# Optimization experiments

Hardware: AMD Instinct MI355X
Metric: run time of the kernel (lower is better)

Reference implementation:

```python
import jax, jax.numpy as jnp
import numpy as np

XYZ_MIN = -1.0
XYZ_MAX = 1.0
ALPHA_INIT = 1e-6
ACT_SHIFT = float(np.log(1.0 / (1.0 - ALPHA_INIT) - 1.0))  # density bias shift


def trilinear_sample(grid, xyz):
    """PyTorch F.grid_sample(mode='bilinear', align_corners=True) for 3D.
    grid: [C, D, H, W] (D<->z, H<->y, W<->x); xyz: [N,3] global coords in [XYZ_MIN, XYZ_MAX].
    Returns [N, C]."""
    C, D, H, W = grid.shape
    u = (xyz - XYZ_MIN) / (XYZ_MAX - XYZ_MIN)            # [N,3] in [0,1]
    sizes = jnp.array([W, H, D], dtype=xyz.dtype)
    pos = u * (sizes - 1.0)                               # align_corners=True mapping
    i0f = jnp.floor(pos)
    w1 = pos - i0f                                        # [N,3] frac weights
    w0 = 1.0 - w1
    maxi = jnp.array([W - 1, H - 1, D - 1], dtype=jnp.int32)
    i0 = jnp.clip(i0f.astype(jnp.int32), 0, maxi)
    i1 = jnp.minimum(i0 + 1, maxi)
    x0, y0, z0 = i0[:, 0], i0[:, 1], i0[:, 2]
    x1, y1, z1 = i1[:, 0], i1[:, 1], i1[:, 2]
    gf = grid.reshape(C, -1)                              # [C, D*H*W]

    def corner(z, y, x):
        lin = (z * H + y) * W + x                         # [N]
        return gf[:, lin]                                 # [C, N]

    wx0, wy0, wz0 = w0[:, 0], w0[:, 1], w0[:, 2]
    wx1, wy1, wz1 = w1[:, 0], w1[:, 1], w1[:, 2]
    out = (corner(z0, y0, x0) * (wz0 * wy0 * wx0)
           + corner(z0, y0, x1) * (wz0 * wy0 * wx1)
           + corner(z0, y1, x0) * (wz0 * wy1 * wx0)
           + corner(z0, y1, x1) * (wz0 * wy1 * wx1)
           + corner(z1, y0, x0) * (wz1 * wy0 * wx0)
           + corner(z1, y0, x1) * (wz1 * wy0 * wx1)
           + corner(z1, y1, x0) * (wz1 * wy1 * wx0)
           + corner(z1, y1, x1) * (wz1 * wy1 * wx1))
    return out.T                                          # [N, C]


def setup_inputs() -> dict:
    key = jax.random.key(0)
    k1, k2, k3, k4, k5 = jax.random.split(key, 5)
    R, P = 16384, 256
    # Keep all sampled points inside [-1, 1]^3 (in-bounds grid_sample).
    origins = (jax.random.uniform(k1, (R, 3), jnp.float32) - 0.5) * 0.5   # [-0.25, 0.25]
    d = jax.random.normal(k2, (R, 3), jnp.float32)
    directions = d / jnp.linalg.norm(d, axis=-1, keepdims=True) * 0.5     # norm 0.5
    lengths = jax.random.uniform(k3, (R, P), jnp.float32)                 # [0, 1)
    density_grid = jax.random.normal(k4, (1, 160, 160, 160), jnp.float32) * 0.1
    color_grid = jax.random.normal(k5, (3, 160, 160, 160), jnp.float32) * 0.1
    return {"origins": origins, "directions": directions, "lengths": lengths,
            "density_grid": density_grid, "color_grid": color_grid}


def reference(origins, directions, lengths, density_grid, color_grid):
    R, P = lengths.shape
    # ray_bundle_to_ray_points: origins + directions * lengths
    pts = origins[:, None, :] + directions[:, None, :] * lengths[:, :, None]  # [R,P,3]
    interval = jnp.linalg.norm(directions, axis=-1)[:, None, None]            # [R,1,1]
    flat = pts.reshape(-1, 3)
    raw_density = trilinear_sample(density_grid, flat).reshape(R, P, 1)
    # alpha = 1 - (1 + exp(density + shift)) ** (-interval)
    density = 1.0 - (1.0 + jnp.exp(raw_density + ACT_SHIFT)) ** (-interval)
    raw_color = trilinear_sample(color_grid, flat).reshape(R, P, 3)
    color = jax.nn.sigmoid(raw_color)
    return density, color
```

## Files before the change

kernel.cpp:

```cpp
#include <hip/hip_runtime.h>
#include <math.h>

#define NRAYS 16384
#define NPTS  256
#define GS    160
#define GS3   (GS*GS*GS)

#define ACT_SHIFT (-13.815509557963774f)
#define LOG2E     (1.4426950408889634f)

typedef float floatx2 __attribute__((ext_vector_type(2)));

__device__ __forceinline__ unsigned int pack4fp8(float d, float r, float g, float b) {
    int w = __builtin_amdgcn_cvt_pk_fp8_f32(d, r, 0, false);
    w     = __builtin_amdgcn_cvt_pk_fp8_f32(g, b, w, true);
    return (unsigned int)w;
}

__device__ __forceinline__ void acc2(unsigned int w, float cw,
                                     floatx2& sdr, floatx2& sgb) {
    floatx2 dr = __builtin_amdgcn_cvt_pk_f32_fp8((int)w, false);
    floatx2 gb = __builtin_amdgcn_cvt_pk_f32_fp8((int)w, true);
    floatx2 cw2 = {cw, cw};
    sdr += dr * cw2;
    sgb += gb * cw2;
}

__global__ __launch_bounds__(256)
void repack_fp8quad_kernel(const float* __restrict__ dgrid,
                           const float* __restrict__ cgrid,
                           uint4* __restrict__ out)
{
    const int i = blockIdx.x * 256 + threadIdx.x;
    if (i >= GS3) return;
    const int x = i % GS;
    const int y = (i / GS) % GS;
    const int ox = (x < GS - 1) ? 1  : 0;
    const int oy = (y < GS - 1) ? GS : 0;

    const int i00 = i, i10 = i + oy, i01 = i + ox, i11 = i + oy + ox;

    uint4 v;
    v.x = pack4fp8(dgrid[i00], cgrid[i00], cgrid[GS3 + i00], cgrid[2*GS3 + i00]);
    v.y = pack4fp8(dgrid[i10], cgrid[i10], cgrid[GS3 + i10], cgrid[2*GS3 + i10]);
    v.z = pack4fp8(dgrid[i01], cgrid[i01], cgrid[GS3 + i01], cgrid[2*GS3 + i01]);
    v.w = pack4fp8(dgrid[i11], cgrid[i11], cgrid[GS3 + i11], cgrid[2*GS3 + i11]);
    out[i] = v;
}

__global__ __launch_bounds__(256)
void sample_fp8_direct_kernel(const float* __restrict__ origins,
                              const float* __restrict__ directions,
                              const float* __restrict__ lengths,
                              const uint4* __restrict__ grid,
                              float* __restrict__ out_density,
                              float* __restrict__ out_color)
{
    const int r   = blockIdx.x;
    const int p   = threadIdx.x;
    const int idx = r * NPTS + p;

    const float t  = lengths[idx];
    const float ox = origins[3*r+0], oy = origins[3*r+1], oz = origins[3*r+2];
    const float dx = directions[3*r+0], dy = directions[3*r+1], dz = directions[3*r+2];
    const float interval = sqrtf(dx*dx + dy*dy + dz*dz);

    const float half_sm1 = 0.5f * (float)(GS - 1);
    const float px = (ox + dx*t + 1.0f) * half_sm1;
    const float py = (oy + dy*t + 1.0f) * half_sm1;
    const float pz = (oz + dz*t + 1.0f) * half_sm1;

    const float fx = floorf(px), fy = floorf(py), fz = floorf(pz);

    int x0 = min(max((int)fx, 0), GS-2);
    int y0 = min(max((int)fy, 0), GS-2);
    int z0 = min(max((int)fz, 0), GS-2);

    const int i0 = (z0*GS + y0)*GS + x0;

    const uint4 ez0 = grid[i0];
    const uint4 ez1 = grid[i0 + GS*GS];

    const float wx1 = px - fx, wy1 = py - fy, wz1 = pz - fz;
    const float wx0 = 1.0f - wx1, wy0 = 1.0f - wy1, wz0 = 1.0f - wz1;
    const float c00 = wy0*wx0, c10 = wy1*wx0, c01 = wy0*wx1, c11 = wy1*wx1;

    floatx2 sdr = {0.f, 0.f}, sgb = {0.f, 0.f};
    acc2(ez0.x, wz0*c00, sdr, sgb);
    acc2(ez0.y, wz0*c10, sdr, sgb);
    acc2(ez0.z, wz0*c01, sdr, sgb);
    acc2(ez0.w, wz0*c11, sdr, sgb);
    acc2(ez1.x, wz1*c00, sdr, sgb);
    acc2(ez1.y, wz1*c10, sdr, sgb);
    acc2(ez1.z, wz1*c01, sdr, sgb);
    acc2(ez1.w, wz1*c11, sdr, sgb);

    const float a  = sdr.x + ACT_SHIFT;
    const float ea = __builtin_amdgcn_exp2f(LOG2E * a);
    const float L  = __builtin_amdgcn_logf(1.0f + ea);
    out_density[idx] = 1.0f - __builtin_amdgcn_exp2f(-interval * L);

    const float e1 = __builtin_amdgcn_exp2f(-LOG2E * sdr.y);
    const float e2 = __builtin_amdgcn_exp2f(-LOG2E * sgb.x);
    const float e3 = __builtin_amdgcn_exp2f(-LOG2E * sgb.y);
    out_color[idx*3 + 0] = __builtin_amdgcn_rcpf(1.0f + e1);
    out_color[idx*3 + 1] = __builtin_amdgcn_rcpf(1.0f + e2);
    out_color[idx*3 + 2] = __builtin_amdgcn_rcpf(1.0f + e3);
}

__device__ __forceinline__ float2 ld2(const float* p) {
    return *reinterpret_cast<const float2*>(p);
}

__global__ __launch_bounds__(256)
void dvgo_render_kernel(const float* __restrict__ origins,
                        const float* __restrict__ directions,
                        const float* __restrict__ lengths,
                        const float* __restrict__ dgrid,
                        const float* __restrict__ cgrid,
                        float* __restrict__ out_density,
                        float* __restrict__ out_color)
{
    const int r = blockIdx.x;
    const int p = threadIdx.x;
    const int idx = r * NPTS + p;

    const float t  = lengths[idx];
    const float ox = origins[3*r+0], oy = origins[3*r+1], oz = origins[3*r+2];
    const float dx = directions[3*r+0], dy = directions[3*r+1], dz = directions[3*r+2];
    const float interval = sqrtf(dx*dx + dy*dy + dz*dz);

    const float x = ox + dx*t;
    const float y = oy + dy*t;
    const float z = oz + dz*t;

    const float half_sm1 = 0.5f * (float)(GS - 1);
    const float px = (x + 1.0f) * half_sm1;
    const float py = (y + 1.0f) * half_sm1;
    const float pz = (z + 1.0f) * half_sm1;

    const float fx = floorf(px), fy = floorf(py), fz = floorf(pz);
    const float wx1 = px - fx, wy1 = py - fy, wz1 = pz - fz;
    const float wx0 = 1.0f - wx1, wy0 = 1.0f - wy1, wz0 = 1.0f - wz1;

    int x0 = (int)fx, y0 = (int)fy, z0 = (int)fz;
    x0 = min(max(x0, 0), GS-2);
    y0 = min(max(y0, 0), GS-2);
    z0 = min(max(z0, 0), GS-2);

    int rows[4];
    rows[0] = ((z0  )*GS + y0  )*GS + x0;
    rows[1] = ((z0  )*GS + y0+1)*GS + x0;
    rows[2] = ((z0+1)*GS + y0  )*GS + x0;
    rows[3] = ((z0+1)*GS + y0+1)*GS + x0;

    const float* bases[4] = {dgrid, cgrid, cgrid + GS3, cgrid + 2*GS3};

    float2 v[4][4];
    #pragma unroll
    for (int ch = 0; ch < 4; ++ch)
        #pragma unroll
        for (int rr = 0; rr < 4; ++rr)
            v[ch][rr] = ld2(bases[ch] + rows[rr]);

    float rw[4];
    rw[0] = wz0*wy0; rw[1] = wz0*wy1; rw[2] = wz1*wy0; rw[3] = wz1*wy1;

    float s[4];
    #pragma unroll
    for (int ch = 0; ch < 4; ++ch) {
        float acc = 0.0f;
        #pragma unroll
        for (int rr = 0; rr < 4; ++rr)
            acc = fmaf(rw[rr], fmaf(v[ch][rr].x, wx0, v[ch][rr].y * wx1), acc);
        s[ch] = acc;
    }

    const float a  = s[0] + ACT_SHIFT;
    const float sp = (a > 20.0f) ? a : log1pf(__expf(a));
    out_density[idx] = 1.0f - __expf(-interval * sp);

    #pragma unroll
    for (int c = 0; c < 3; ++c)
        out_color[idx*3 + c] = 1.0f / (1.0f + __expf(-s[c+1]));
}

extern "C" void kernel_launch(void* const* d_in, const int* in_sizes, int n_in,
                              void* d_out, int out_size, void* d_ws, size_t ws_size,
                              hipStream_t stream) {
    const float* origins    = (const float*)d_in[0];
    const float* directions = (const float*)d_in[1];
    const float* lengths    = (const float*)d_in[2];
    const float* dgrid      = (const float*)d_in[3];
    const float* cgrid      = (const float*)d_in[4];

    float* out_density = (float*)d_out;
    float* out_color   = (float*)d_out + NRAYS*NPTS;

    if (ws_size >= (size_t)GS3 * sizeof(uint4)) {
        uint4* quads = (uint4*)d_ws;
        repack_fp8quad_kernel<<<(GS3 + 255) / 256, 256, 0, stream>>>(dgrid, cgrid, quads);
        sample_fp8_direct_kernel<<<NRAYS, NPTS, 0, stream>>>(
            origins, directions, lengths, quads, out_density, out_color);
    } else {
        dvgo_render_kernel<<<NRAYS, NPTS, 0, stream>>>(
            origins, directions, lengths, dgrid, cgrid, out_density, out_color);
    }
}
```

Before: 56.22 us.

## Repack grid as fp8 y-pairs and read x-neighbors with one 16-byte load

The repacked fp8 grid now stores only the voxel and its y+1 neighbor per entry, as 8 bytes, instead of a 16-byte quad that also held the x+1 neighbors. The sampler gets all four corners of a z-slice with one 16-byte load covering two adjacent entries. This halves both the repack write traffic and the workspace footprint, which should improve cache reuse during sampling. It also switches the lengths load and the output stores to nontemporal hints. The 16-byte loads are now only 8-byte aligned.

```diff
diff --git a/kernel.cpp b/kernel.cpp
--- a/kernel.cpp
+++ b/kernel.cpp
@@ -27,40 +27,34 @@
 }
 
 __global__ __launch_bounds__(256)
-void repack_fp8quad_kernel(const float* __restrict__ dgrid,
-                           const float* __restrict__ cgrid,
-                           uint4* __restrict__ out)
+void repack_fp8ypair_kernel(const float* __restrict__ dgrid,
+                            const float* __restrict__ cgrid,
+                            uint2* __restrict__ out)
 {
     const int i = blockIdx.x * 256 + threadIdx.x;
     if (i >= GS3) return;
-    const int x = i % GS;
-    const int y = (i / GS) % GS;
-    const int ox = (x < GS - 1) ? 1  : 0;
-    const int oy = (y < GS - 1) ? GS : 0;
-
-    const int i00 = i, i10 = i + oy, i01 = i + ox, i11 = i + oy + ox;
-
-    uint4 v;
-    v.x = pack4fp8(dgrid[i00], cgrid[i00], cgrid[GS3 + i00], cgrid[2*GS3 + i00]);
-    v.y = pack4fp8(dgrid[i10], cgrid[i10], cgrid[GS3 + i10], cgrid[2*GS3 + i10]);
-    v.z = pack4fp8(dgrid[i01], cgrid[i01], cgrid[GS3 + i01], cgrid[2*GS3 + i01]);
-    v.w = pack4fp8(dgrid[i11], cgrid[i11], cgrid[GS3 + i11], cgrid[2*GS3 + i11]);
+    const int y  = (i / GS) % GS;
+    const int iy = (y < GS - 1) ? i + GS : i;
+
+    uint2 v;
+    v.x = pack4fp8(dgrid[i],  cgrid[i],  cgrid[GS3 + i],  cgrid[2*GS3 + i]);
+    v.y = pack4fp8(dgrid[iy], cgrid[iy], cgrid[GS3 + iy], cgrid[2*GS3 + iy]);
     out[i] = v;
 }
 
 __global__ __launch_bounds__(256)
-void sample_fp8_direct_kernel(const float* __restrict__ origins,
-                              const float* __restrict__ directions,
-                              const float* __restrict__ lengths,
-                              const uint4* __restrict__ grid,
-                              float* __restrict__ out_density,
-                              float* __restrict__ out_color)
+void sample_fp8yp_kernel(const float* __restrict__ origins,
+                         const float* __restrict__ directions,
+                         const float* __restrict__ lengths,
+                         const uint2* __restrict__ grid,
+                         float* __restrict__ out_density,
+                         float* __restrict__ out_color)
 {
     const int r   = blockIdx.x;
     const int p   = threadIdx.x;
     const int idx = r * NPTS + p;
 
-    const float t  = lengths[idx];
+    const float t  = __builtin_nontemporal_load(&lengths[idx]);
     const float ox = origins[3*r+0], oy = origins[3*r+1], oz = origins[3*r+2];
     const float dx = directions[3*r+0], dy = directions[3*r+1], dz = directions[3*r+2];
     const float interval = sqrtf(dx*dx + dy*dy + dz*dz);
@@ -78,8 +72,8 @@
 
     const int i0 = (z0*GS + y0)*GS + x0;
 
-    const uint4 ez0 = grid[i0];
-    const uint4 ez1 = grid[i0 + GS*GS];
+    const uint4 ez0 = *reinterpret_cast<const uint4*>(&grid[i0]);
+    const uint4 ez1 = *reinterpret_cast<const uint4*>(&grid[i0 + GS*GS]);
 
     const float wx1 = px - fx, wy1 = py - fy, wz1 = pz - fz;
     const float wx0 = 1.0f - wx1, wy0 = 1.0f - wy1, wz0 = 1.0f - wz1;
@@ -98,14 +92,15 @@
     const float a  = sdr.x + ACT_SHIFT;
     const float ea = __builtin_amdgcn_exp2f(LOG2E * a);
     const float L  = __builtin_amdgcn_logf(1.0f + ea);
-    out_density[idx] = 1.0f - __builtin_amdgcn_exp2f(-interval * L);
+    __builtin_nontemporal_store(1.0f - __builtin_amdgcn_exp2f(-interval * L),
+                                &out_density[idx]);
 
     const float e1 = __builtin_amdgcn_exp2f(-LOG2E * sdr.y);
     const float e2 = __builtin_amdgcn_exp2f(-LOG2E * sgb.x);
     const float e3 = __builtin_amdgcn_exp2f(-LOG2E * sgb.y);
-    out_color[idx*3 + 0] = __builtin_amdgcn_rcpf(1.0f + e1);
-    out_color[idx*3 + 1] = __builtin_amdgcn_rcpf(1.0f + e2);
-    out_color[idx*3 + 2] = __builtin_amdgcn_rcpf(1.0f + e3);
+    __builtin_nontemporal_store(__builtin_amdgcn_rcpf(1.0f + e1), &out_color[idx*3 + 0]);
+    __builtin_nontemporal_store(__builtin_amdgcn_rcpf(1.0f + e2), &out_color[idx*3 + 1]);
+    __builtin_nontemporal_store(__builtin_amdgcn_rcpf(1.0f + e3), &out_color[idx*3 + 2]);
 }
 
 __device__ __forceinline__ float2 ld2(const float* p) {
@@ -197,11 +192,11 @@
     float* out_density = (float*)d_out;
     float* out_color   = (float*)d_out + NRAYS*NPTS;
 
-    if (ws_size >= (size_t)GS3 * sizeof(uint4)) {
-        uint4* quads = (uint4*)d_ws;
-        repack_fp8quad_kernel<<<(GS3 + 255) / 256, 256, 0, stream>>>(dgrid, cgrid, quads);
-        sample_fp8_direct_kernel<<<NRAYS, NPTS, 0, stream>>>(
-            origins, directions, lengths, quads, out_density, out_color);
+    if (ws_size >= (size_t)GS3 * sizeof(uint2)) {
+        uint2* ypairs = (uint2*)d_ws;
+        repack_fp8ypair_kernel<<<(GS3 + 255) / 256, 256, 0, stream>>>(dgrid, cgrid, ypairs);
+        sample_fp8yp_kernel<<<NRAYS, NPTS, 0, stream>>>(
+            origins, directions, lengths, ypairs, out_density, out_color);
     } else {
         dvgo_render_kernel<<<NRAYS, NPTS, 0, stream>>>(
             origins, directions, lengths, dgrid, cgrid, out_density, out_color);
```

New measurement: 56.47 us. About the same (+0.4%).
